# Performance work log

Hardware: AMD Instinct MI355X
Metric: run time of the kernel (lower is better)

Reference implementation:

```python
import jax, jax.numpy as jnp
import numpy as np

B, S, D_IN = 4, 2048, 1024
EMBED, HEADS = 1024, 16
HEAD_DIM = EMBED // HEADS


def setup_inputs() -> dict:
    key = jax.random.key(0)
    k1, k2, k3 = jax.random.split(key, 3)
    x = jax.random.normal(k1, (B, S, D_IN), dtype=jnp.float32)
    # xavier-uniform-ish init scales
    lim_qkv = float(np.sqrt(6.0 / (D_IN + 3 * EMBED)))
    lim_o = float(np.sqrt(6.0 / (EMBED + EMBED)))
    w_qkv = jax.random.uniform(k2, (3 * EMBED, D_IN), minval=-lim_qkv, maxval=lim_qkv, dtype=jnp.float32)
    b_qkv = jnp.zeros((3 * EMBED,), dtype=jnp.float32)
    w_o = jax.random.uniform(k3, (EMBED, EMBED), minval=-lim_o, maxval=lim_o, dtype=jnp.float32)
    b_o = jnp.zeros((EMBED,), dtype=jnp.float32)
    return {"x": x, "w_qkv": w_qkv, "b_qkv": b_qkv, "w_o": w_o, "b_o": b_o}


def reference(x, w_qkv, b_qkv, w_o, b_o):
    b, s, _ = x.shape
    qkv = jnp.einsum('bsi,oi->bso', x, w_qkv) + b_qkv            # (b, s, 3E)
    qkv = qkv.reshape(b, s, HEADS, 3 * HEAD_DIM).transpose(0, 2, 1, 3)  # (b, h, s, 3d)
    q, k, v = jnp.split(qkv, 3, axis=-1)                          # each (b, h, s, d)
    scale = 1.0 / jnp.sqrt(jnp.float32(HEAD_DIM))
    attn = jnp.einsum('bhqd,bhkd->bhqk', q, k) * scale            # (b, h, s, s)
    attn = jax.nn.softmax(attn, axis=-1)
    vals = jnp.einsum('bhqk,bhkd->bhqd', attn, v)                 # (b, h, s, d)
    # NOTE: original torch code reshapes (b,h,s,d) -> (b,s,e) WITHOUT transposing
    # heads back; jnp.reshape reproduces that flattening exactly.
    vals = vals.reshape(b, s, EMBED)
    out = jnp.einsum('bse,oe->bso', vals, w_o) + b_o              # (b, s, E)
    return out
```

## Files before the change

### kernel.cpp

```cpp
#include <hip/hip_runtime.h>
#include <stdint.h>
#include <stddef.h>

#define DEVINL __device__ __forceinline__

typedef unsigned short u16;
typedef unsigned int u32;
typedef __attribute__((ext_vector_type(8))) short short8;
typedef __attribute__((ext_vector_type(4))) float f32x4;
typedef __attribute__((ext_vector_type(4))) u32 u32x4;
typedef __attribute__((ext_vector_type(2))) u32 u32x2;

#define QSCALE 0.18033688011112042f

DEVINL u16 f2bf(float f) {
    u32 u = __builtin_bit_cast(u32, f);
    u32 r = (u + 0x7fffu + ((u >> 16) & 1u)) >> 16;
    return (u16)r;
}

DEVINL void gld_lds16(const void* g, void* l) {
    __builtin_amdgcn_global_load_lds(
        (__attribute__((address_space(1))) u32*)(uintptr_t)g,
        (__attribute__((address_space(3))) u32*)l, 16, 0, 0);
}

DEVINL u32 pack_bf16_trunc(float lo, float hi) {
    return __builtin_amdgcn_perm(__builtin_bit_cast(u32, hi),
                                 __builtin_bit_cast(u32, lo), 0x07060302u);
}

__global__ void cast_f32_bf16(const float* __restrict__ in, u16* __restrict__ out) {
    int i = (blockIdx.x * 256 + threadIdx.x) * 8;
    float4 a = *(const float4*)(in + i);
    float4 c = *(const float4*)(in + i + 4);
    union { u16 s[8]; u32x4 v; } t;
    t.s[0] = f2bf(a.x); t.s[1] = f2bf(a.y); t.s[2] = f2bf(a.z); t.s[3] = f2bf(a.w);
    t.s[4] = f2bf(c.x); t.s[5] = f2bf(c.y); t.s[6] = f2bf(c.z); t.s[7] = f2bf(c.w);
    *(u32x4*)(out + i) = t.v;
}

__global__ void cast_wqkv(const float* __restrict__ in, u16* __restrict__ out) {
    int i = (blockIdx.x * 256 + threadIdx.x) * 8;
    int row = i >> 10;
    float sc = ((row % 192) < 64) ? QSCALE : 1.0f;
    float4 a = *(const float4*)(in + i);
    float4 c = *(const float4*)(in + i + 4);
    union { u16 s[8]; u32x4 v; } t;
    t.s[0] = f2bf(a.x * sc); t.s[1] = f2bf(a.y * sc); t.s[2] = f2bf(a.z * sc); t.s[3] = f2bf(a.w * sc);
    t.s[4] = f2bf(c.x * sc); t.s[5] = f2bf(c.y * sc); t.s[6] = f2bf(c.z * sc); t.s[7] = f2bf(c.w * sc);
    *(u32x4*)(out + i) = t.v;
}

__global__ void scale_bqkv(const float* __restrict__ in, float* __restrict__ out) {
    int i = blockIdx.x * 256 + threadIdx.x;
    float sc = ((i % 192) < 64) ? QSCALE : 1.0f;
    out[i] = in[i] * sc;
}

template <int OUT_BF16>
__global__ void gemm_abt(const u16* __restrict__ A, const u16* __restrict__ Bm,
                         const float* __restrict__ bias, void* __restrict__ Cout,
                         int M, int N, int K) {
    __shared__ u16 As[128 * 32];
    __shared__ u16 Bs[128 * 32];
    const int tid = threadIdx.x;
    const int lane = tid & 63;
    const int wv = tid >> 6, wr = wv >> 1, wc = wv & 1;
    const int l15 = lane & 15, quad = lane >> 4;
    const int m0 = blockIdx.y * 128, n0 = blockIdx.x * 128;

    f32x4 acc[4][4];
#pragma unroll
    for (int i = 0; i < 4; i++)
#pragma unroll
        for (int j = 0; j < 4; j++) acc[i][j] = (f32x4){0.f, 0.f, 0.f, 0.f};

    const u16* Ab = A + (size_t)m0 * K;
    const u16* Bb = Bm + (size_t)n0 * K;
    const int srow = tid >> 2;
    const int sc8 = (tid & 3) * 8;

    for (int k0 = 0; k0 < K; k0 += 32) {
#pragma unroll
        for (int i = 0; i < 2; i++) {
            int row = i * 64 + srow;
            gld_lds16(Ab + (size_t)row * K + k0 + sc8, (char*)As + (size_t)(i * 256 + tid) * 16);
            gld_lds16(Bb + (size_t)row * K + k0 + sc8, (char*)Bs + (size_t)(i * 256 + tid) * 16);
        }
        __syncthreads();
        short8 af[4], bf8[4];
#pragma unroll
        for (int mi = 0; mi < 4; mi++)
            af[mi] = *(const short8*)(As + (wr * 64 + mi * 16 + l15) * 32 + quad * 8);
#pragma unroll
        for (int ni = 0; ni < 4; ni++)
            bf8[ni] = *(const short8*)(Bs + (wc * 64 + ni * 16 + l15) * 32 + quad * 8);
#pragma unroll
        for (int mi = 0; mi < 4; mi++)
#pragma unroll
            for (int ni = 0; ni < 4; ni++)
                acc[mi][ni] = __builtin_amdgcn_mfma_f32_16x16x32_bf16(af[mi], bf8[ni], acc[mi][ni], 0, 0, 0);
        __syncthreads();
    }

#pragma unroll
    for (int mi = 0; mi < 4; mi++) {
        int row_b = m0 + wr * 64 + mi * 16 + quad * 4;
#pragma unroll
        for (int ni = 0; ni < 4; ni++) {
            int col = n0 + wc * 64 + ni * 16 + l15;
            float bv = bias[col];
#pragma unroll
            for (int r = 0; r < 4; r++) {
                float v = acc[mi][ni][r] + bv;
                size_t idx = (size_t)(row_b + r) * N + col;
                if (OUT_BF16) ((u16*)Cout)[idx] = f2bf(v);
                else          ((float*)Cout)[idx] = v;
            }
        }
    }
}

__global__ void transpose_v(const u16* __restrict__ qkv, u16* __restrict__ vtb) {
    __shared__ u16 Vl[64][72];
    const int tid = threadIdx.x;
    const int s0 = blockIdx.x * 64;
    const int bh = blockIdx.y, b = bh >> 4, h = bh & 15;
    const u16* src = qkv + (size_t)(b * 2048 + s0) * 3072 + h * 192 + 128;
#pragma unroll
    for (int i = 0; i < 2; i++) {
        int cid = i * 256 + tid;
        int rs = cid >> 3, c8 = (cid & 7) * 8;
        *(u32x4*)(&Vl[rs][c8]) = *(const u32x4*)(src + (size_t)rs * 3072 + c8);
    }
    __syncthreads();
#pragma unroll
    for (int i = 0; i < 2; i++) {
        int cid = i * 256 + tid;
        int d = cid >> 3, sc = cid & 7;
        union { u16 s[8]; u32x4 v; } t;
#pragma unroll
        for (int j = 0; j < 8; j++) t.s[j] = Vl[sc * 8 + j][d];
        *(u32x4*)(vtb + ((size_t)bh * 64 + d) * 2048 + s0 + sc * 8) = t.v;
    }
}

__launch_bounds__(256, 4)
__global__ void flash_attn(const u16* __restrict__ qkv, const u16* __restrict__ vt,
                           u16* __restrict__ vals2) {
    __shared__ u16 Ks[64 * 72];
    __shared__ u16 Vts[64 * 72];
    __shared__ u16 Ps[4][32 * 72];

    const int tid = threadIdx.x;
    const int lane = tid & 63, wv = tid >> 6;
    const int l15 = lane & 15, quad = lane >> 4;
    const int s0 = blockIdx.x * 128;
    const int bh = blockIdx.y, b = bh >> 4, h = bh & 15;

    short8 qf[2][2];
    const u16* qbase = qkv + (size_t)(b * 2048 + s0 + wv * 32) * 3072 + h * 192;
#pragma unroll
    for (int qi = 0; qi < 2; qi++)
#pragma unroll
        for (int ks = 0; ks < 2; ks++)
            qf[qi][ks] = *(const short8*)(qbase + (size_t)(qi * 16 + l15) * 3072 + ks * 32 + quad * 8);

    f32x4 o_acc[2][4];
    f32x4 sum_acc[2];
#pragma unroll
    for (int qi = 0; qi < 2; qi++) {
        sum_acc[qi] = (f32x4){0.f, 0.f, 0.f, 0.f};
#pragma unroll
        for (int nd = 0; nd < 4; nd++) o_acc[qi][nd] = (f32x4){0.f, 0.f, 0.f, 0.f};
    }

    const u16* kg = qkv + (size_t)(b * 2048) * 3072 + h * 192 + 64;
    const u16* vg = vt + (size_t)bh * 64 * 2048;
    const int srow = tid >> 2;
    const int sc16 = (tid & 3) * 16;

    const short8 ones = (short8){0x3F80, 0x3F80, 0x3F80, 0x3F80, 0x3F80, 0x3F80, 0x3F80, 0x3F80};

    for (int kb = 0; kb < 2048; kb += 64) {
        __syncthreads();
        u32x4 k0 = *(const u32x4*)(kg + (size_t)(kb + srow) * 3072 + sc16);
        u32x4 k1 = *(const u32x4*)(kg + (size_t)(kb + srow) * 3072 + sc16 + 8);
        u32x4 v0 = *(const u32x4*)(vg + (size_t)srow * 2048 + kb + sc16);
        u32x4 v1 = *(const u32x4*)(vg + (size_t)srow * 2048 + kb + sc16 + 8);
        *(u32x4*)(Ks + srow * 72 + sc16) = k0;
        *(u32x4*)(Ks + srow * 72 + sc16 + 8) = k1;
        *(u32x4*)(Vts + srow * 72 + sc16) = v0;
        *(u32x4*)(Vts + srow * 72 + sc16 + 8) = v1;
        __syncthreads();

        f32x4 s_acc[4][2];
#pragma unroll
        for (int ki = 0; ki < 4; ki++)
#pragma unroll
            for (int qi = 0; qi < 2; qi++) s_acc[ki][qi] = (f32x4){0.f, 0.f, 0.f, 0.f};
#pragma unroll
        for (int ki = 0; ki < 4; ki++) {
#pragma unroll
            for (int ks = 0; ks < 2; ks++) {
                short8 kf = *(const short8*)(Ks + (ki * 16 + l15) * 72 + ks * 32 + quad * 8);
#pragma unroll
                for (int qi = 0; qi < 2; qi++)
                    s_acc[ki][qi] = __builtin_amdgcn_mfma_f32_16x16x32_bf16(kf, qf[qi][ks], s_acc[ki][qi], 0, 0, 0);
            }
        }

#pragma unroll
        for (int ki = 0; ki < 4; ki++)
#pragma unroll
            for (int qi = 0; qi < 2; qi++) {
                float p0 = __builtin_amdgcn_exp2f(s_acc[ki][qi][0]);
                float p1 = __builtin_amdgcn_exp2f(s_acc[ki][qi][1]);
                float p2 = __builtin_amdgcn_exp2f(s_acc[ki][qi][2]);
                float p3 = __builtin_amdgcn_exp2f(s_acc[ki][qi][3]);
                u32x2 pk = (u32x2){pack_bf16_trunc(p0, p1), pack_bf16_trunc(p2, p3)};
                *(u32x2*)(Ps[wv] + (qi * 16 + l15) * 72 + ki * 16 + quad * 4) = pk;
            }

#pragma unroll
        for (int c = 0; c < 2; c++) {
            short8 ap[2];
#pragma unroll
            for (int qi = 0; qi < 2; qi++)
                ap[qi] = *(const short8*)(Ps[wv] + (qi * 16 + l15) * 72 + c * 32 + quad * 8);
#pragma unroll
            for (int qi = 0; qi < 2; qi++)
                sum_acc[qi] = __builtin_amdgcn_mfma_f32_16x16x32_bf16(ap[qi], ones, sum_acc[qi], 0, 0, 0);
#pragma unroll
            for (int nd = 0; nd < 4; nd++) {
                short8 bv = *(const short8*)(Vts + (nd * 16 + l15) * 72 + c * 32 + quad * 8);
#pragma unroll
                for (int qi = 0; qi < 2; qi++)
                    o_acc[qi][nd] = __builtin_amdgcn_mfma_f32_16x16x32_bf16(ap[qi], bv, o_acc[qi][nd], 0, 0, 0);
            }
        }
    }

#pragma unroll
    for (int qi = 0; qi < 2; qi++) {
        f32x4 inv;
#pragma unroll
        for (int r = 0; r < 4; r++) inv[r] = 1.0f / sum_acc[qi][r];
#pragma unroll
        for (int nd = 0; nd < 4; nd++) {
            int d = nd * 16 + l15;
#pragma unroll
            for (int r = 0; r < 4; r++) {
                int s = s0 + wv * 32 + qi * 16 + quad * 4 + r;
                size_t row2 = (size_t)(b * 2048 + h * 128 + (s >> 4));
                int col2 = ((s & 15) << 6) + d;
                vals2[row2 * 1024 + col2] = f2bf(o_acc[qi][nd][r] * inv[r]);
            }
        }
    }
}

extern "C" void kernel_launch(void* const* d_in, const int* in_sizes, int n_in,
                              void* d_out, int out_size, void* d_ws, size_t ws_size,
                              hipStream_t stream) {
    (void)in_sizes; (void)n_in; (void)out_size; (void)ws_size;
    const float* x      = (const float*)d_in[0];
    const float* w_qkv  = (const float*)d_in[1];
    const float* b_qkv  = (const float*)d_in[2];
    const float* w_o    = (const float*)d_in[3];
    const float* b_o    = (const float*)d_in[4];
    float* out = (float*)d_out;

    char* ws = (char*)d_ws;
    u16* xb   = (u16*)(ws);
    u16* wqb  = (u16*)(ws + 16777216);
    u16* wob  = (u16*)(ws + 23068672);
    u16* qkvb = (u16*)(ws + 25165824);
    u16* vtb  = (u16*)(ws + 75497472);
    u16* v2b  = (u16*)(ws + 92274688);
    float* bsc = (float*)(ws + 75497472);

    cast_f32_bf16<<<4096, 256, 0, stream>>>(x, xb);
    cast_wqkv<<<1536, 256, 0, stream>>>(w_qkv, wqb);
    cast_f32_bf16<<<512, 256, 0, stream>>>(w_o, wob);
    scale_bqkv<<<12, 256, 0, stream>>>(b_qkv, bsc);

    gemm_abt<1><<<dim3(24, 64), 256, 0, stream>>>(xb, wqb, bsc, qkvb, 8192, 3072, 1024);

    transpose_v<<<dim3(32, 64), 256, 0, stream>>>(qkvb, vtb);

    flash_attn<<<dim3(16, 64), 256, 0, stream>>>(qkvb, vtb, v2b);

    gemm_abt<0><<<dim3(8, 64), 256, 0, stream>>>(v2b, wob, b_o, out, 8192, 1024, 1024);
}
```

Before: 289.8 us.

## Fuse input casts into one kernel; stream K via direct LDS loads, V from global

Merges the four input-preparation kernels into a single launch to cut launch overhead. In flash attention, K tiles are now 128 rows per iteration, loaded with global_load_lds into a XOR-swizzled unpadded LDS layout, which halves the number of block barriers. V fragments are read straight from global memory (the pre-transposed V) instead of being staged in LDS. This frees LDS but makes the PV MFMAs depend on global-load latency, with possible cache traffic from the uncoalesced per-lane V reads.

Measured after the change: 332.4 us. 14.7% more time.

```diff
diff --git a/kernel.cpp b/kernel.cpp
--- a/kernel.cpp
+++ b/kernel.cpp
@@ -30,32 +30,30 @@
                                  __builtin_bit_cast(u32, lo), 0x07060302u);
 }
 
-__global__ void cast_f32_bf16(const float* __restrict__ in, u16* __restrict__ out) {
-    int i = (blockIdx.x * 256 + threadIdx.x) * 8;
-    float4 a = *(const float4*)(in + i);
-    float4 c = *(const float4*)(in + i + 4);
-    union { u16 s[8]; u32x4 v; } t;
-    t.s[0] = f2bf(a.x); t.s[1] = f2bf(a.y); t.s[2] = f2bf(a.z); t.s[3] = f2bf(a.w);
-    t.s[4] = f2bf(c.x); t.s[5] = f2bf(c.y); t.s[6] = f2bf(c.z); t.s[7] = f2bf(c.w);
-    *(u32x4*)(out + i) = t.v;
-}
-
-__global__ void cast_wqkv(const float* __restrict__ in, u16* __restrict__ out) {
-    int i = (blockIdx.x * 256 + threadIdx.x) * 8;
-    int row = i >> 10;
-    float sc = ((row % 192) < 64) ? QSCALE : 1.0f;
-    float4 a = *(const float4*)(in + i);
-    float4 c = *(const float4*)(in + i + 4);
-    union { u16 s[8]; u32x4 v; } t;
-    t.s[0] = f2bf(a.x * sc); t.s[1] = f2bf(a.y * sc); t.s[2] = f2bf(a.z * sc); t.s[3] = f2bf(a.w * sc);
-    t.s[4] = f2bf(c.x * sc); t.s[5] = f2bf(c.y * sc); t.s[6] = f2bf(c.z * sc); t.s[7] = f2bf(c.w * sc);
-    *(u32x4*)(out + i) = t.v;
-}
-
-__global__ void scale_bqkv(const float* __restrict__ in, float* __restrict__ out) {
-    int i = blockIdx.x * 256 + threadIdx.x;
-    float sc = ((i % 192) < 64) ? QSCALE : 1.0f;
-    out[i] = in[i] * sc;
+__global__ void prep_inputs(const float* __restrict__ x, const float* __restrict__ wqkv,
+                            const float* __restrict__ bqkv, const float* __restrict__ wo,
+                            u16* __restrict__ xb, u16* __restrict__ wqb,
+                            u16* __restrict__ wob, float* __restrict__ bsc) {
+    int blk = blockIdx.x;
+    if (blk < 6144) {
+        const float* src; u16* dst; int base; bool qscale = false;
+        if (blk < 4096)      { src = x;    dst = xb;  base = blk; }
+        else if (blk < 5632) { src = wqkv; dst = wqb; base = blk - 4096; qscale = true; }
+        else                 { src = wo;   dst = wob; base = blk - 5632; }
+        int i = (base * 256 + threadIdx.x) * 8;
+        float sc = 1.0f;
+        if (qscale) { int row = i >> 10; if ((row % 192) < 64) sc = QSCALE; }
+        float4 a = *(const float4*)(src + i);
+        float4 c = *(const float4*)(src + i + 4);
+        union { u16 s[8]; u32x4 v; } t;
+        t.s[0] = f2bf(a.x * sc); t.s[1] = f2bf(a.y * sc); t.s[2] = f2bf(a.z * sc); t.s[3] = f2bf(a.w * sc);
+        t.s[4] = f2bf(c.x * sc); t.s[5] = f2bf(c.y * sc); t.s[6] = f2bf(c.z * sc); t.s[7] = f2bf(c.w * sc);
+        *(u32x4*)(dst + i) = t.v;
+    } else {
+        int i = (blk - 6144) * 256 + threadIdx.x;
+        float sc = ((i % 192) < 64) ? QSCALE : 1.0f;
+        bsc[i] = bqkv[i] * sc;
+    }
 }
 
 template <int OUT_BF16>
@@ -149,8 +147,7 @@
 __launch_bounds__(256, 4)
 __global__ void flash_attn(const u16* __restrict__ qkv, const u16* __restrict__ vt,
                            u16* __restrict__ vals2) {
-    __shared__ u16 Ks[64 * 72];
-    __shared__ u16 Vts[64 * 72];
+    __shared__ u16 Ks[128 * 64];
     __shared__ u16 Ps[4][32 * 72];
 
     const int tid = threadIdx.x;
@@ -178,66 +175,76 @@
 
     const u16* kg = qkv + (size_t)(b * 2048) * 3072 + h * 192 + 64;
     const u16* vg = vt + (size_t)bh * 64 * 2048;
-    const int srow = tid >> 2;
-    const int sc16 = (tid & 3) * 16;
+
+    int srcoff[4]; int dstoff[4];
+#pragma unroll
+    for (int i = 0; i < 4; i++) {
+        int t = i * 256 + tid;
+        int row = t >> 3;
+        int c = (t & 7) ^ (row & 7);
+        srcoff[i] = row * 3072 + c * 8;
+        dstoff[i] = (i * 256 + wv * 64) * 16;
+    }
 
     const short8 ones = (short8){0x3F80, 0x3F80, 0x3F80, 0x3F80, 0x3F80, 0x3F80, 0x3F80, 0x3F80};
 
-    for (int kb = 0; kb < 2048; kb += 64) {
+    for (int kb = 0; kb < 2048; kb += 128) {
         __syncthreads();
-        u32x4 k0 = *(const u32x4*)(kg + (size_t)(kb + srow) * 3072 + sc16);
-        u32x4 k1 = *(const u32x4*)(kg + (size_t)(kb + srow) * 3072 + sc16 + 8);
-        u32x4 v0 = *(const u32x4*)(vg + (size_t)srow * 2048 + kb + sc16);
-        u32x4 v1 = *(const u32x4*)(vg + (size_t)srow * 2048 + kb + sc16 + 8);
-        *(u32x4*)(Ks + srow * 72 + sc16) = k0;
-        *(u32x4*)(Ks + srow * 72 + sc16 + 8) = k1;
-        *(u32x4*)(Vts + srow * 72 + sc16) = v0;
-        *(u32x4*)(Vts + srow * 72 + sc16 + 8) = v1;
+#pragma unroll
+        for (int i = 0; i < 4; i++)
+            gld_lds16(kg + (size_t)kb * 3072 + srcoff[i], (char*)Ks + dstoff[i]);
         __syncthreads();
 
-        f32x4 s_acc[4][2];
-#pragma unroll
-        for (int ki = 0; ki < 4; ki++)
-#pragma unroll
-            for (int qi = 0; qi < 2; qi++) s_acc[ki][qi] = (f32x4){0.f, 0.f, 0.f, 0.f};
-#pragma unroll
-        for (int ki = 0; ki < 4; ki++) {
-#pragma unroll
-            for (int ks = 0; ks < 2; ks++) {
-                short8 kf = *(const short8*)(Ks + (ki * 16 + l15) * 72 + ks * 32 + quad * 8);
+#pragma unroll
+        for (int sub = 0; sub < 2; sub++) {
+            f32x4 s_acc[4][2];
+#pragma unroll
+            for (int ki = 0; ki < 4; ki++)
+#pragma unroll
+                for (int qi = 0; qi < 2; qi++) s_acc[ki][qi] = (f32x4){0.f, 0.f, 0.f, 0.f};
+#pragma unroll
+            for (int ki = 0; ki < 4; ki++) {
+#pragma unroll
+                for (int ks = 0; ks < 2; ks++) {
+                    short8 kf = *(const short8*)(Ks + (sub * 64 + ki * 16 + l15) * 64 +
+                                                 (((ks * 4 + quad) ^ (l15 & 7)) * 8));
+#pragma unroll
+                    for (int qi = 0; qi < 2; qi++)
+                        s_acc[ki][qi] = __builtin_amdgcn_mfma_f32_16x16x32_bf16(kf, qf[qi][ks], s_acc[ki][qi], 0, 0, 0);
+                }
+            }
+
+#pragma unroll
+            for (int ki = 0; ki < 4; ki++)
+#pragma unroll
+                for (int qi = 0; qi < 2; qi++) {
+                    float p0 = __builtin_amdgcn_exp2f(s_acc[ki][qi][0]);
+                    float p1 = __builtin_amdgcn_exp2f(s_acc[ki][qi][1]);
+                    float p2 = __builtin_amdgcn_exp2f(s_acc[ki][qi][2]);
+                    float p3 = __builtin_amdgcn_exp2f(s_acc[ki][qi][3]);
+                    u32x2 pk = (u32x2){pack_bf16_trunc(p0, p1), pack_bf16_trunc(p2, p3)};
+                    *(u32x2*)(Ps[wv] + (qi * 16 + l15) * 72 + ki * 16 + quad * 4) = pk;
+                }
+
+#pragma unroll
+            for (int c = 0; c < 2; c++) {
+                short8 vf[4];
+#pragma unroll
+                for (int nd = 0; nd < 4; nd++)
+                    vf[nd] = *(const short8*)(vg + (size_t)(nd * 16 + l15) * 2048 +
+                                              kb + sub * 64 + c * 32 + quad * 8);
+                short8 ap[2];
 #pragma unroll
                 for (int qi = 0; qi < 2; qi++)
-                    s_acc[ki][qi] = __builtin_amdgcn_mfma_f32_16x16x32_bf16(kf, qf[qi][ks], s_acc[ki][qi], 0, 0, 0);
-            }
-        }
-
-#pragma unroll
-        for (int ki = 0; ki < 4; ki++)
-#pragma unroll
-            for (int qi = 0; qi < 2; qi++) {
-                float p0 = __builtin_amdgcn_exp2f(s_acc[ki][qi][0]);
-                float p1 = __builtin_amdgcn_exp2f(s_acc[ki][qi][1]);
-                float p2 = __builtin_amdgcn_exp2f(s_acc[ki][qi][2]);
-                float p3 = __builtin_amdgcn_exp2f(s_acc[ki][qi][3]);
-                u32x2 pk = (u32x2){pack_bf16_trunc(p0, p1), pack_bf16_trunc(p2, p3)};
-                *(u32x2*)(Ps[wv] + (qi * 16 + l15) * 72 + ki * 16 + quad * 4) = pk;
-            }
-
-#pragma unroll
-        for (int c = 0; c < 2; c++) {
-            short8 ap[2];
-#pragma unroll
-            for (int qi = 0; qi < 2; qi++)
-                ap[qi] = *(const short8*)(Ps[wv] + (qi * 16 + l15) * 72 + c * 32 + quad * 8);
-#pragma unroll
-            for (int qi = 0; qi < 2; qi++)
-                sum_acc[qi] = __builtin_amdgcn_mfma_f32_16x16x32_bf16(ap[qi], ones, sum_acc[qi], 0, 0, 0);
-#pragma unroll
-            for (int nd = 0; nd < 4; nd++) {
-                short8 bv = *(const short8*)(Vts + (nd * 16 + l15) * 72 + c * 32 + quad * 8);
+                    ap[qi] = *(const short8*)(Ps[wv] + (qi * 16 + l15) * 72 + c * 32 + quad * 8);
 #pragma unroll
                 for (int qi = 0; qi < 2; qi++)
-                    o_acc[qi][nd] = __builtin_amdgcn_mfma_f32_16x16x32_bf16(ap[qi], bv, o_acc[qi][nd], 0, 0, 0);
+                    sum_acc[qi] = __builtin_amdgcn_mfma_f32_16x16x32_bf16(ap[qi], ones, sum_acc[qi], 0, 0, 0);
+#pragma unroll
+                for (int nd = 0; nd < 4; nd++)
+#pragma unroll
+                    for (int qi = 0; qi < 2; qi++)
+                        o_acc[qi][nd] = __builtin_amdgcn_mfma_f32_16x16x32_bf16(ap[qi], vf[nd], o_acc[qi][nd], 0, 0, 0);
             }
         }
     }
@@ -281,10 +288,7 @@
     u16* v2b  = (u16*)(ws + 92274688);
     float* bsc = (float*)(ws + 75497472);
 
-    cast_f32_bf16<<<4096, 256, 0, stream>>>(x, xb);
-    cast_wqkv<<<1536, 256, 0, stream>>>(w_qkv, wqb);
-    cast_f32_bf16<<<512, 256, 0, stream>>>(w_o, wob);
-    scale_bqkv<<<12, 256, 0, stream>>>(b_qkv, bsc);
+    prep_inputs<<<6156, 256, 0, stream>>>(x, w_qkv, b_qkv, w_o, xb, wqb, wob, bsc);
 
     gemm_abt<1><<<dim3(24, 64), 256, 0, stream>>>(xb, wqb, bsc, qkvb, 8192, 3072, 1024);
 
```
